# Kernel optimization log

Hardware: AMD Instinct MI355X
Metric: run time of the kernel (lower is better)

The kernel has to match this reference:

```python
import jax, jax.numpy as jnp
import numpy as np

B, L, HID = 2, 2048, 2560
H, HKV, DH = 32, 8, 128
G = H // HKV  # GQA groups = 4
EPS = 1e-6
THETA = 1000000.0


def setup_inputs() -> dict:
    key = jax.random.key(0)
    ks = jax.random.split(key, 6)
    x = jax.random.normal(ks[0], (B, L, HID), dtype=jnp.float32)
    Wq = jax.random.normal(ks[1], (HID, H * DH), dtype=jnp.float32) * 0.02
    Wk = jax.random.normal(ks[2], (HID, HKV * DH), dtype=jnp.float32) * 0.02
    Wv = jax.random.normal(ks[3], (HID, HKV * DH), dtype=jnp.float32) * 0.02
    Wo = jax.random.normal(ks[4], (H * DH, HID), dtype=jnp.float32) * 0.02
    q_norm_w = jnp.ones((DH,), dtype=jnp.float32)
    k_norm_w = jnp.ones((DH,), dtype=jnp.float32)
    # RoPE tables, theta=1e6, non-interleaved (half-split) layout
    inv_freq = 1.0 / (THETA ** (jnp.arange(0, DH, 2, dtype=jnp.float32) / DH))
    pos = jnp.arange(L, dtype=jnp.float32)
    freqs = pos[:, None] * inv_freq[None, :]              # [L, DH/2]
    emb = jnp.concatenate([freqs, freqs], axis=-1)        # [L, DH]
    cos = jnp.broadcast_to(jnp.cos(emb)[None], (B, L, DH))
    sin = jnp.broadcast_to(jnp.sin(emb)[None], (B, L, DH))
    return {"x": x, "Wq": Wq, "Wk": Wk, "Wv": Wv, "Wo": Wo,
            "q_norm_w": q_norm_w, "k_norm_w": k_norm_w,
            "cos": cos, "sin": sin}


def _rmsnorm(x, w):
    xf = x.astype(jnp.float32)
    var = jnp.mean(xf * xf, axis=-1, keepdims=True)
    return (xf * jax.lax.rsqrt(var + EPS)).astype(x.dtype) * w


def _rotate_half(x):
    x1, x2 = jnp.split(x, 2, axis=-1)
    return jnp.concatenate([-x2, x1], axis=-1)


def reference(x, Wq, Wk, Wv, Wo, q_norm_w, k_norm_w, cos, sin):
    b, l, _ = x.shape
    q = (x @ Wq).reshape(b, l, H, DH)
    k = (x @ Wk).reshape(b, l, HKV, DH)
    v = (x @ Wv).reshape(b, l, HKV, DH).transpose(0, 2, 1, 3)   # [B,HKV,L,DH]
    q = _rmsnorm(q, q_norm_w).transpose(0, 2, 1, 3)             # [B,H,L,DH]
    k = _rmsnorm(k, k_norm_w).transpose(0, 2, 1, 3)             # [B,HKV,L,DH]
    c = cos[:, None]  # [B,1,L,DH]
    s = sin[:, None]
    q = q * c + _rotate_half(q) * s
    k = k * c + _rotate_half(k) * s
    # GQA SDPA, causal
    qg = q.reshape(b, HKV, G, l, DH)
    scale = 1.0 / np.sqrt(DH)
    scores = jnp.einsum('bkgqd,bkmd->bkgqm', qg, k) * scale     # [B,HKV,G,L,L]
    causal = jnp.tril(jnp.ones((l, l), dtype=bool))
    scores = jnp.where(causal, scores, jnp.finfo(scores.dtype).min)
    attn = jax.nn.softmax(scores, axis=-1)
    out = jnp.einsum('bkgqm,bkmd->bkgqd', attn, v)              # [B,HKV,G,L,DH]
    out = out.reshape(b, H, l, DH).transpose(0, 2, 1, 3).reshape(b, l, H * DH)
    return out @ Wo
```

## Files before the change

### kernel.cpp

```cpp
#include <hip/hip_runtime.h>

typedef unsigned short u16;
typedef unsigned int u32;
using bf16x8 = __attribute__((ext_vector_type(8))) __bf16;
using f32x4  = __attribute__((ext_vector_type(4))) float;

typedef const void __attribute__((address_space(1)))* gas1p;
typedef void __attribute__((address_space(3)))* las3p;

__device__ __forceinline__ void gload16(const void* g, void* l) {
  __builtin_amdgcn_global_load_lds((gas1p)g, (las3p)l, 16, 0, 0);
}

__device__ __forceinline__ u16 f2bf(float f) {
  union { float f; unsigned u; } v; v.f = f;
  unsigned r = v.u + 0x7FFFu + ((v.u >> 16) & 1u);
  return (u16)(r >> 16);
}
__device__ __forceinline__ float bf2f(u16 h) {
  union { unsigned u; float f; } v; v.u = ((unsigned)h) << 16;
  return v.f;
}

__global__ __launch_bounds__(256)
void cvt_f32_bf16(const float4* __restrict__ in, uint2* __restrict__ out, int n4) {
  int i = blockIdx.x * 256 + threadIdx.x;
  if (i >= n4) return;
  float4 v = in[i];
  uint2 o;
  o.x = (unsigned)f2bf(v.x) | ((unsigned)f2bf(v.y) << 16);
  o.y = (unsigned)f2bf(v.z) | ((unsigned)f2bf(v.w) << 16);
  out[i] = o;
}

__global__ __launch_bounds__(256)
void transpose_all(const float* __restrict__ Wq, const float* __restrict__ Wk,
                   const float* __restrict__ Wv, const float* __restrict__ Wo,
                   u16* __restrict__ WqkvT, u16* __restrict__ WoT) {
  __shared__ float tile[32][33];
  const int bid = blockIdx.x;
  const float* in; u16* out; int C, R, bx, by;
  if (bid < 10240)      { in = Wq; out = WqkvT;                         R = 2560; C = 4096; bx = bid % 128;           by = bid / 128; }
  else if (bid < 12800) { in = Wk; out = WqkvT + (size_t)4096 * 2560;   R = 2560; C = 1024; bx = (bid - 10240) % 32;  by = (bid - 10240) / 32; }
  else if (bid < 15360) { in = Wv; out = WqkvT + (size_t)5120 * 2560;   R = 2560; C = 1024; bx = (bid - 12800) % 32;  by = (bid - 12800) / 32; }
  else                  { in = Wo; out = WoT;                           R = 4096; C = 2560; bx = (bid - 15360) % 80;  by = (bid - 15360) / 80; }
  const int tx = threadIdx.x & 31, ty = threadIdx.x >> 5;
  const int r0 = by * 32, c0 = bx * 32;
#pragma unroll
  for (int i = 0; i < 4; i++)
    tile[ty + i * 8][tx] = in[(size_t)(r0 + ty + i * 8) * C + c0 + tx];
  __syncthreads();
#pragma unroll
  for (int i = 0; i < 4; i++)
    out[(size_t)(c0 + ty + i * 8) * R + r0 + tx] = f2bf(tile[tx][ty + i * 8]);
}

__global__ __launch_bounds__(256)
void transpose_v(const u16* __restrict__ QKV, u16* __restrict__ Vt) {
  __shared__ u16 tile[32][34];
  const int tx = threadIdx.x & 31, ty = threadIdx.x >> 5;
  const int l0 = blockIdx.x * 32, d0 = blockIdx.y * 32;
  const int bkv = blockIdx.z;
  const int b = bkv >> 3, kvh = bkv & 7;
#pragma unroll
  for (int i = 0; i < 4; i++)
    tile[ty + i * 8][tx] =
        QKV[(size_t)(b * 2048 + l0 + ty + i * 8) * 6144 + 5120 + kvh * 128 + d0 + tx];
  __syncthreads();
#pragma unroll
  for (int i = 0; i < 4; i++)
    Vt[((size_t)bkv * 128 + d0 + ty + i * 8) * 2048 + l0 + tx] = tile[tx][ty + i * 8];
}

__global__ __launch_bounds__(256)
void norm_rope(const u16* __restrict__ QKV, const float* __restrict__ qw,
               const float* __restrict__ kw, const float* __restrict__ cosp,
               const float* __restrict__ sinp, u16* __restrict__ Qr,
               u16* __restrict__ Kr) {
  const int rid = blockIdx.x * 4 + (threadIdx.x >> 6);
  const int lane = threadIdx.x & 63;
  const int head = rid % 40;
  const int bl = rid / 40;
  const int b = bl >> 11, l = bl & 2047;
  const u16* src; const float* w; u16* dst; float scale;
  if (head < 32) {
    src = QKV + (size_t)bl * 6144 + head * 128;
    w = qw;
    dst = Qr + ((size_t)(b * 32 + head) * 2048 + l) * 128;
    scale = 0.08838834764831845f;
  } else {
    const int kvh = head - 32;
    src = QKV + (size_t)bl * 6144 + 4096 + kvh * 128;
    w = kw;
    dst = Kr + ((size_t)(b * 8 + kvh) * 2048 + l) * 128;
    scale = 1.0f;
  }
  float lo = bf2f(src[lane]);
  float hi = bf2f(src[lane + 64]);
  float ss = lo * lo + hi * hi;
#pragma unroll
  for (int m = 1; m < 64; m <<= 1) ss += __shfl_xor(ss, m, 64);
  const float rstd = rsqrtf(ss * (1.0f / 128.0f) + 1e-6f) * scale;
  const float nlo = lo * rstd * w[lane];
  const float nhi = hi * rstd * w[lane + 64];
  const float* cb = cosp + (size_t)bl * 128;
  const float* sb = sinp + (size_t)bl * 128;
  dst[lane]      = f2bf(nlo * cb[lane]      - nhi * sb[lane]);
  dst[lane + 64] = f2bf(nhi * cb[lane + 64] + nlo * sb[lane + 64]);
}

#define BAR __builtin_amdgcn_s_barrier()
#define WLG { asm volatile("s_waitcnt lgkmcnt(0)" ::: "memory");            \
              __builtin_amdgcn_sched_barrier(0); }
#define WVMn(n) asm volatile("s_waitcnt vmcnt(" #n ")" ::: "memory")
#define SP1 __builtin_amdgcn_s_setprio(1)
#define SP0 __builtin_amdgcn_s_setprio(0)

template <int MINW, int BM, int BN, int WM, int WN, typename CT>
__global__ __launch_bounds__(512, MINW)
void gemmT(const u16* __restrict__ A, const u16* __restrict__ Bt,
           CT* __restrict__ C, int N, int K, int MT) {
  extern __shared__ char smem[];
  constexpr int ASZ = BM * 128;
  constexpr int BSZ = BN * 128;
  constexpr int MI = BM / WM / 16;
  constexpr int NJF = BN / WN / 16;
  constexpr int NL = BM / 64 + (BN + 63) / 64;
  const int tid = threadIdx.x, lane = tid & 63, wid = tid >> 6;
  const int wm = wid / WN, wn = wid % WN;
  const int fr = lane & 15, fq = lane >> 4;
  const int qx = (int)gridDim.x >> 3;
  const int wg = ((int)blockIdx.x & 7) * qx + ((int)blockIdx.x >> 3);
  const int bx = wg / MT, by = wg - bx * MT;
  const int m0 = by * BM, n0 = bx * BN;
  const u16* Ab = A + (size_t)m0 * K;
  const u16* Bb = Bt + (size_t)n0 * K;

#define ABUF(c) (smem + (c) * ASZ)
#define BBUF(c) (smem + 2 * ASZ + (c) * BSZ)

  f32x4 acc[MI][NJF];
#pragma unroll
  for (int i = 0; i < MI; i++)
#pragma unroll
    for (int j = 0; j < NJF; j++)
#pragma unroll
      for (int r = 0; r < 4; r++) acc[i][j][r] = 0.f;

  auto stage = [&](int c, int kk) {
#pragma unroll
    for (int l = 0; l < BM / 64; l++) {
      const int u = tid + 512 * l, row = u >> 3, ch = u & 7;
      gload16(Ab + (size_t)row * K + ((ch ^ (row & 7)) << 3) + kk,
              ABUF(c) + (u << 4));
    }
#pragma unroll
    for (int l = 0; l < BN / 64; l++) {
      const int u = tid + 512 * l, row = u >> 3, ch = u & 7;
      gload16(Bb + (size_t)row * K + ((ch ^ (row & 7)) << 3) + kk,
              BBUF(c) + (u << 4));
    }
    if constexpr ((BN % 64) != 0) {
      const int u = (BN / 64) * 512 + (tid & 255), row = u >> 3, ch = u & 7;
      gload16(Bb + (size_t)row * K + ((ch ^ (row & 7)) << 3) + kk,
              BBUF(c) + (u << 4));
    }
  };

  const int NT = K >> 6;
  stage(0, 0);
  stage(1, 64);
  if constexpr (NL == 5) { WVMn(5); } else { WVMn(7); }
  BAR;

  bf16x8 af[MI][2], bf[NJF][2];
  for (int t = 0; t < NT; t++) {
    const int c = t & 1;
#pragma unroll
    for (int i = 0; i < MI; i++) {
      const int row = (wm * MI + i) * 16 + fr;
#pragma unroll
      for (int ks = 0; ks < 2; ks++)
        af[i][ks] = *(const bf16x8*)(ABUF(c) + row * 128 +
                                     ((((ks << 2) + fq) ^ (row & 7)) << 4));
    }
#pragma unroll
    for (int j = 0; j < NJF; j++) {
      const int row = (j * WN + wn) * 16 + fr;
#pragma unroll
      for (int ks = 0; ks < 2; ks++)
        bf[j][ks] = *(const bf16x8*)(BBUF(c) + row * 128 +
                                     ((((ks << 2) + fq) ^ (row & 7)) << 4));
    }
    WLG;
    BAR;
    int t2 = t + 2; if (t2 >= NT) t2 -= NT;
    stage(c, t2 << 6);
    if constexpr (NL == 5) { WVMn(5); } else { WVMn(7); }
    SP1;
#pragma unroll
    for (int j = 0; j < NJF; j++)
#pragma unroll
      for (int i = 0; i < MI; i++) {
        acc[i][j] = __builtin_amdgcn_mfma_f32_16x16x32_bf16(af[i][0], bf[j][0],
                                                            acc[i][j], 0, 0, 0);
        acc[i][j] = __builtin_amdgcn_mfma_f32_16x16x32_bf16(af[i][1], bf[j][1],
                                                            acc[i][j], 0, 0, 0);
      }
    SP0;
    BAR;
  }
  WVMn(0);

#pragma unroll
  for (int i = 0; i < MI; i++) {
    const int row0 = m0 + (wm * MI + i) * 16 + fq * 4;
#pragma unroll
    for (int j = 0; j < NJF; j++) {
      const int col = n0 + (j * WN + wn) * 16 + fr;
#pragma unroll
      for (int r = 0; r < 4; r++) {
        const size_t idx = (size_t)(row0 + r) * N + col;
        if constexpr (sizeof(CT) == 2) C[idx] = f2bf(acc[i][j][r]);
        else C[idx] = acc[i][j][r];
      }
    }
  }
#undef ABUF
#undef BBUF
}

__global__ __launch_bounds__(256, 2)
void attn_fwd(const u16* __restrict__ Qr, const u16* __restrict__ Kr,
              const u16* __restrict__ Vt, u16* __restrict__ AO) {
  const int L = 2048, DH = 128;
  __shared__ u16 Ks[2][64 * 128];
  __shared__ u16 Vs[2][128 * 64];
  const int tid = threadIdx.x, lane = tid & 63, wid = tid >> 6;
  const int fr = lane & 15, fq = lane >> 4;
  const int j = blockIdx.x >> 4;
  const int grp = blockIdx.x & 15;
  const int kvh = grp >> 1, b = grp & 1;
  const int h = kvh * 4 + wid;

  const u16* Kbase = Kr + (size_t)(b * 8 + kvh) * L * DH;
  const u16* Vbase = Vt + (size_t)(b * 8 + kvh) * DH * L;

  int Dly[4], kOff[4], vOff[4];
#pragma unroll
  for (int p = 0; p < 4; p++) {
    const int D = (tid + p * 256) * 16;
    Dly[p] = D;
    const int kr = D >> 8, kc = ((D >> 4) & 15) ^ (kr & 7);
    kOff[p] = kr * 128 + kc * 8;
    const int vr = D >> 7, vc = ((D >> 4) & 7) ^ (vr & 7);
    vOff[p] = vr * 2048 + vc * 8;
  }

  auto stage = [&](int kt, int bufi) {
    const int k0 = kt * 64;
#pragma unroll
    for (int p = 0; p < 4; p++) {
      gload16(Kbase + (size_t)k0 * 128 + kOff[p], (char*)&Ks[bufi][0] + Dly[p]);
      gload16(Vbase + k0 + vOff[p], (char*)&Vs[bufi][0] + Dly[p]);
    }
  };

  for (int half = 0; half < 2; half++) {
    const int t = half ? 63 - j : j;
    const int nk = (t >> 1) + 1;

    bf16x8 qf[2][4];
#pragma unroll
    for (int g = 0; g < 2; g++) {
      const int qq = t * 32 + g * 16 + fr;
      const u16* qbase = Qr + ((size_t)(b * 32 + h) * L + qq) * DH + fq * 8;
#pragma unroll
      for (int dt = 0; dt < 4; dt++) qf[g][dt] = *(const bf16x8*)(qbase + dt * 32);
    }
    asm volatile("s_waitcnt vmcnt(0)" ::: "memory");

    f32x4 o[2][8];
#pragma unroll
    for (int g = 0; g < 2; g++)
#pragma unroll
      for (int d = 0; d < 8; d++)
#pragma unroll
        for (int r = 0; r < 4; r++) o[g][d][r] = 0.f;
    float mrow[2] = {-__builtin_huge_valf(), -__builtin_huge_valf()};
    float lrow[2] = {0.f, 0.f};

    __builtin_amdgcn_s_barrier();
    stage(0, 0);
    int cur = 0;

    for (int kt = 0; kt < nk; kt++) {
      if (kt + 1 < nk) {
        stage(kt + 1, cur ^ 1);
        asm volatile("s_waitcnt vmcnt(8)" ::: "memory");
      } else {
        asm volatile("s_waitcnt vmcnt(0)" ::: "memory");
      }
      __builtin_amdgcn_s_barrier();

      const u16* KsB = &Ks[cur][0];
      const u16* VsB = &Vs[cur][0];
      const int k0 = kt * 64;

      f32x4 s4[2][4];
#pragma unroll
      for (int g = 0; g < 2; g++)
#pragma unroll
        for (int ni = 0; ni < 4; ni++)
#pragma unroll
          for (int r = 0; r < 4; r++) s4[g][ni][r] = 0.f;
      SP1;
#pragma unroll
      for (int ni = 0; ni < 4; ni++) {
        const int krow = ni * 16 + fr;
        const int sw = (krow & 7) << 4;
#pragma unroll
        for (int dt = 0; dt < 4; dt++) {
          const int off = (krow * 256 + dt * 64 + fq * 16) ^ sw;
          bf16x8 kf = *(const bf16x8*)((const char*)KsB + off);
          s4[0][ni] = __builtin_amdgcn_mfma_f32_16x16x32_bf16(kf, qf[0][dt], s4[0][ni], 0, 0, 0);
          s4[1][ni] = __builtin_amdgcn_mfma_f32_16x16x32_bf16(kf, qf[1][dt], s4[1][ni], 0, 0, 0);
        }
      }
      SP0;

      if (kt == nk - 1) {
#pragma unroll
        for (int g = 0; g < 2; g++) {
          const int qq = t * 32 + g * 16 + fr;
#pragma unroll
          for (int ni = 0; ni < 4; ni++)
#pragma unroll
            for (int r = 0; r < 4; r++)
              if (k0 + ni * 16 + fq * 4 + r > qq) s4[g][ni][r] = -1e30f;
        }
      }

      bf16x8 pb[2][2];
#pragma unroll
      for (int g = 0; g < 2; g++) {
        float m0t = fmaxf(fmaxf(s4[g][0][0], s4[g][0][1]), fmaxf(s4[g][0][2], s4[g][0][3]));
        float m1t = fmaxf(fmaxf(s4[g][1][0], s4[g][1][1]), fmaxf(s4[g][1][2], s4[g][1][3]));
        float m2t = fmaxf(fmaxf(s4[g][2][0], s4[g][2][1]), fmaxf(s4[g][2][2], s4[g][2][3]));
        float m3t = fmaxf(fmaxf(s4[g][3][0], s4[g][3][1]), fmaxf(s4[g][3][2], s4[g][3][3]));
        float mt = fmaxf(fmaxf(m0t, m1t), fmaxf(m2t, m3t));
        mt = fmaxf(mt, __shfl_xor(mt, 16, 64));
        mt = fmaxf(mt, __shfl_xor(mt, 32, 64));

        if (!__all(mt <= mrow[g] + 8.f)) {
          const float mn = fmaxf(mrow[g], mt);
          const float corr = exp2f((mrow[g] - mn) * 1.44269504f);
          mrow[g] = mn;
          lrow[g] *= corr;
#pragma unroll
          for (int d = 0; d < 8; d++)
#pragma unroll
            for (int r = 0; r < 4; r++) o[g][d][r] *= corr;
        }

        const float ml = mrow[g] * 1.44269504f;
        float rp[4] = {0.f, 0.f, 0.f, 0.f};
#pragma unroll
        for (int ni = 0; ni < 4; ni++)
#pragma unroll
          for (int r = 0; r < 4; r++) {
            const float pv = exp2f(fmaf(s4[g][ni][r], 1.44269504f, -ml));
            s4[g][ni][r] = pv;
            rp[r] += pv;
          }
        float rs = (rp[0] + rp[1]) + (rp[2] + rp[3]);
        rs += __shfl_xor(rs, 16, 64);
        rs += __shfl_xor(rs, 32, 64);
        lrow[g] += rs;

        u32 pk[4][2];
#pragma unroll
        for (int ni = 0; ni < 4; ni++) {
          pk[ni][0] = __builtin_amdgcn_perm(__float_as_uint(s4[g][ni][1]),
                                            __float_as_uint(s4[g][ni][0]), 0x07060302u);
          pk[ni][1] = __builtin_amdgcn_perm(__float_as_uint(s4[g][ni][3]),
                                            __float_as_uint(s4[g][ni][2]), 0x07060302u);
        }
#pragma unroll
        for (int ks = 0; ks < 2; ks++) {
          auto s0 = __builtin_amdgcn_permlane32_swap(pk[2 * ks + 0][0],
                                                     pk[2 * ks + 1][0], false, false);
          auto s1 = __builtin_amdgcn_permlane32_swap(pk[2 * ks + 0][1],
                                                     pk[2 * ks + 1][1], false, false);
          auto q0 = __builtin_amdgcn_permlane16_swap(s0[0], s0[1], false, false);
          auto q1 = __builtin_amdgcn_permlane16_swap(s1[0], s1[1], false, false);
          union { u32 u[4]; bf16x8 v; } pbv;
          pbv.u[0] = q0[0]; pbv.u[1] = q1[0]; pbv.u[2] = q0[1]; pbv.u[3] = q1[1];
          pb[g][ks] = pbv.v;
        }
      }

      SP1;
#pragma unroll
      for (int d = 0; d < 8; d++) {
        const int vrow = d * 16 + fr;
        const int sw = (vrow & 7) << 4;
#pragma unroll
        for (int ks = 0; ks < 2; ks++) {
          const int off = (vrow * 128 + ks * 64 + fq * 16) ^ sw;
          bf16x8 vf = *(const bf16x8*)((const char*)VsB + off);
          o[0][d] = __builtin_amdgcn_mfma_f32_16x16x32_bf16(vf, pb[0][ks], o[0][d], 0, 0, 0);
          o[1][d] = __builtin_amdgcn_mfma_f32_16x16x32_bf16(vf, pb[1][ks], o[1][d], 0, 0, 0);
        }
      }
      SP0;
      __builtin_amdgcn_s_barrier();
      cur ^= 1;
    }

#pragma unroll
    for (int g = 0; g < 2; g++) {
      const float inv = 1.f / lrow[g];
      const int qq = t * 32 + g * 16 + fr;
      u16* obase = AO + ((size_t)b * L + qq) * 4096 + h * 128 + fq * 4;
#pragma unroll
      for (int d = 0; d < 8; d++) {
        uint2 w;
        w.x = (u32)f2bf(o[g][d][0] * inv) | ((u32)f2bf(o[g][d][1] * inv) << 16);
        w.y = (u32)f2bf(o[g][d][2] * inv) | ((u32)f2bf(o[g][d][3] * inv) << 16);
        *(uint2*)(obase + d * 16) = w;
      }
    }
  }
}

extern "C" void kernel_launch(void* const* d_in, const int* in_sizes, int n_in,
                              void* d_out, int out_size, void* d_ws, size_t ws_size,
                              hipStream_t stream) {
  const float* x    = (const float*)d_in[0];
  const float* Wq   = (const float*)d_in[1];
  const float* Wk   = (const float*)d_in[2];
  const float* Wv   = (const float*)d_in[3];
  const float* Wo   = (const float*)d_in[4];
  const float* qw   = (const float*)d_in[5];
  const float* kw   = (const float*)d_in[6];
  const float* cosp = (const float*)d_in[7];
  const float* sinp = (const float*)d_in[8];
  float* out = (float*)d_out;
  char* ws = (char*)d_ws;

  u16* xb    = (u16*)(ws);
  u16* WqkvT = (u16*)(ws + 20971520);
  u16* WoT   = (u16*)(ws + 52428800);
  u16* QKV   = (u16*)(ws + 73400320);
  u16* AO    = QKV;
  u16* Qrr   = (u16*)(ws + 123731968);
  u16* Krr   = (u16*)(ws + 157286400);
  u16* Vtt   = (u16*)(ws + 165675008);

  hipFuncSetAttribute(reinterpret_cast<const void*>(&gemmT<4, 128, 192, 2, 4, u16>),
                      hipFuncAttributeMaxDynamicSharedMemorySize, 81920);
  hipFuncSetAttribute(reinterpret_cast<const void*>(&gemmT<2, 256, 160, 4, 2, float>),
                      hipFuncAttributeMaxDynamicSharedMemorySize, 106496);

  cvt_f32_bf16<<<10240, 256, 0, stream>>>((const float4*)x, (uint2*)xb, 2621440);
  transpose_all<<<25600, 256, 0, stream>>>(Wq, Wk, Wv, Wo, WqkvT, WoT);

  gemmT<4, 128, 192, 2, 4, u16><<<1024, 512, 81920, stream>>>(xb, WqkvT, QKV, 6144, 2560, 32);

  norm_rope<<<40960, 256, 0, stream>>>(QKV, qw, kw, cosp, sinp, Qrr, Krr);
  transpose_v<<<dim3(64, 4, 16), 256, 0, stream>>>(QKV, Vtt);

  attn_fwd<<<dim3(512), 256, 0, stream>>>(Qrr, Krr, Vtt, AO);

  gemmT<2, 256, 160, 4, 2, float><<<256, 512, 106496, stream>>>(AO, WoT, out, 2560, 4096, 16);
}
```

Measured before the change: 408.4 us.

## Split attention into one tile per block, read V directly, retile output GEMM

```diff
diff --git a/kernel.cpp b/kernel.cpp
--- a/kernel.cpp
+++ b/kernel.cpp
@@ -230,206 +230,191 @@
 #undef BBUF
 }
 
-__global__ __launch_bounds__(256, 2)
+__global__ __launch_bounds__(256, 4)
 void attn_fwd(const u16* __restrict__ Qr, const u16* __restrict__ Kr,
               const u16* __restrict__ Vt, u16* __restrict__ AO) {
   const int L = 2048, DH = 128;
   __shared__ u16 Ks[2][64 * 128];
-  __shared__ u16 Vs[2][128 * 64];
   const int tid = threadIdx.x, lane = tid & 63, wid = tid >> 6;
   const int fr = lane & 15, fq = lane >> 4;
-  const int j = blockIdx.x >> 4;
+  const int t = 63 - (int)(blockIdx.x >> 4);
   const int grp = blockIdx.x & 15;
   const int kvh = grp >> 1, b = grp & 1;
   const int h = kvh * 4 + wid;
+  const int nk = (t >> 1) + 1;
 
   const u16* Kbase = Kr + (size_t)(b * 8 + kvh) * L * DH;
   const u16* Vbase = Vt + (size_t)(b * 8 + kvh) * DH * L;
 
-  int Dly[4], kOff[4], vOff[4];
+  int Dly[4], kOff[4];
 #pragma unroll
   for (int p = 0; p < 4; p++) {
     const int D = (tid + p * 256) * 16;
     Dly[p] = D;
     const int kr = D >> 8, kc = ((D >> 4) & 15) ^ (kr & 7);
     kOff[p] = kr * 128 + kc * 8;
-    const int vr = D >> 7, vc = ((D >> 4) & 7) ^ (vr & 7);
-    vOff[p] = vr * 2048 + vc * 8;
-  }
-
-  auto stage = [&](int kt, int bufi) {
+  }
+
+  auto stageK = [&](int kt, int bufi) {
     const int k0 = kt * 64;
 #pragma unroll
-    for (int p = 0; p < 4; p++) {
+    for (int p = 0; p < 4; p++)
       gload16(Kbase + (size_t)k0 * 128 + kOff[p], (char*)&Ks[bufi][0] + Dly[p]);
-      gload16(Vbase + k0 + vOff[p], (char*)&Vs[bufi][0] + Dly[p]);
-    }
   };
 
-  for (int half = 0; half < 2; half++) {
-    const int t = half ? 63 - j : j;
-    const int nk = (t >> 1) + 1;
-
-    bf16x8 qf[2][4];
+  bf16x8 qf[2][4];
+#pragma unroll
+  for (int g = 0; g < 2; g++) {
+    const int qq = t * 32 + g * 16 + fr;
+    const u16* qbase = Qr + ((size_t)(b * 32 + h) * L + qq) * DH + fq * 8;
+#pragma unroll
+    for (int dt = 0; dt < 4; dt++) qf[g][dt] = *(const bf16x8*)(qbase + dt * 32);
+  }
+
+  f32x4 o[2][8];
+#pragma unroll
+  for (int g = 0; g < 2; g++)
+#pragma unroll
+    for (int d = 0; d < 8; d++)
+#pragma unroll
+      for (int r = 0; r < 4; r++) o[g][d][r] = 0.f;
+  float mrow[2] = {-__builtin_huge_valf(), -__builtin_huge_valf()};
+  float lrow[2] = {0.f, 0.f};
+
+  stageK(0, 0);
+  asm volatile("s_waitcnt vmcnt(0)" ::: "memory");
+  __builtin_amdgcn_s_barrier();
+  int cur = 0;
+
+  for (int kt = 0; kt < nk; kt++) {
+    if (kt + 1 < nk) stageK(kt + 1, cur ^ 1);
+
+    const u16* KsB = &Ks[cur][0];
+    const int k0 = kt * 64;
+
+    f32x4 s4[2][4];
+#pragma unroll
+    for (int g = 0; g < 2; g++)
+#pragma unroll
+      for (int ni = 0; ni < 4; ni++)
+#pragma unroll
+        for (int r = 0; r < 4; r++) s4[g][ni][r] = 0.f;
+    SP1;
+#pragma unroll
+    for (int ni = 0; ni < 4; ni++) {
+      const int krow = ni * 16 + fr;
+      const int sw = (krow & 7) << 4;
+#pragma unroll
+      for (int dt = 0; dt < 4; dt++) {
+        const int off = (krow * 256 + dt * 64 + fq * 16) ^ sw;
+        bf16x8 kf = *(const bf16x8*)((const char*)KsB + off);
+        s4[0][ni] = __builtin_amdgcn_mfma_f32_16x16x32_bf16(kf, qf[0][dt], s4[0][ni], 0, 0, 0);
+        s4[1][ni] = __builtin_amdgcn_mfma_f32_16x16x32_bf16(kf, qf[1][dt], s4[1][ni], 0, 0, 0);
+      }
+    }
+    SP0;
+
+    if (kt == nk - 1) {
+#pragma unroll
+      for (int g = 0; g < 2; g++) {
+        const int qq = t * 32 + g * 16 + fr;
+#pragma unroll
+        for (int ni = 0; ni < 4; ni++)
+#pragma unroll
+          for (int r = 0; r < 4; r++)
+            if (k0 + ni * 16 + fq * 4 + r > qq) s4[g][ni][r] = -1e30f;
+      }
+    }
+
+    bf16x8 pb[2][2];
 #pragma unroll
     for (int g = 0; g < 2; g++) {
-      const int qq = t * 32 + g * 16 + fr;
-      const u16* qbase = Qr + ((size_t)(b * 32 + h) * L + qq) * DH + fq * 8;
-#pragma unroll
-      for (int dt = 0; dt < 4; dt++) qf[g][dt] = *(const bf16x8*)(qbase + dt * 32);
-    }
+      float m0t = fmaxf(fmaxf(s4[g][0][0], s4[g][0][1]), fmaxf(s4[g][0][2], s4[g][0][3]));
+      float m1t = fmaxf(fmaxf(s4[g][1][0], s4[g][1][1]), fmaxf(s4[g][1][2], s4[g][1][3]));
+      float m2t = fmaxf(fmaxf(s4[g][2][0], s4[g][2][1]), fmaxf(s4[g][2][2], s4[g][2][3]));
+      float m3t = fmaxf(fmaxf(s4[g][3][0], s4[g][3][1]), fmaxf(s4[g][3][2], s4[g][3][3]));
+      float mt = fmaxf(fmaxf(m0t, m1t), fmaxf(m2t, m3t));
+      mt = fmaxf(mt, __shfl_xor(mt, 16, 64));
+      mt = fmaxf(mt, __shfl_xor(mt, 32, 64));
+
+      if (!__all(mt <= mrow[g] + 8.f)) {
+        const float mn = fmaxf(mrow[g], mt);
+        const float corr = exp2f((mrow[g] - mn) * 1.44269504f);
+        mrow[g] = mn;
+        lrow[g] *= corr;
+#pragma unroll
+        for (int d = 0; d < 8; d++)
+#pragma unroll
+          for (int r = 0; r < 4; r++) o[g][d][r] *= corr;
+      }
+
+      const float ml = mrow[g] * 1.44269504f;
+      float rp[4] = {0.f, 0.f, 0.f, 0.f};
+#pragma unroll
+      for (int ni = 0; ni < 4; ni++)
+#pragma unroll
+        for (int r = 0; r < 4; r++) {
+          const float pv = exp2f(fmaf(s4[g][ni][r], 1.44269504f, -ml));
+          s4[g][ni][r] = pv;
+          rp[r] += pv;
+        }
+      float rs = (rp[0] + rp[1]) + (rp[2] + rp[3]);
+      rs += __shfl_xor(rs, 16, 64);
+      rs += __shfl_xor(rs, 32, 64);
+      lrow[g] += rs;
+
+      u32 pk[4][2];
+#pragma unroll
+      for (int ni = 0; ni < 4; ni++) {
+        pk[ni][0] = __builtin_amdgcn_perm(__float_as_uint(s4[g][ni][1]),
+                                          __float_as_uint(s4[g][ni][0]), 0x07060302u);
+        pk[ni][1] = __builtin_amdgcn_perm(__float_as_uint(s4[g][ni][3]),
+                                          __float_as_uint(s4[g][ni][2]), 0x07060302u);
+      }
+#pragma unroll
+      for (int ks = 0; ks < 2; ks++) {
+        auto s0 = __builtin_amdgcn_permlane32_swap(pk[2 * ks + 0][0],
+                                                   pk[2 * ks + 1][0], false, false);
+        auto s1 = __builtin_amdgcn_permlane32_swap(pk[2 * ks + 0][1],
+                                                   pk[2 * ks + 1][1], false, false);
+        auto q0 = __builtin_amdgcn_permlane16_swap(s0[0], s0[1], false, false);
+        auto q1 = __builtin_amdgcn_permlane16_swap(s1[0], s1[1], false, false);
+        union { u32 u[4]; bf16x8 v; } pbv;
+        pbv.u[0] = q0[0]; pbv.u[1] = q1[0]; pbv.u[2] = q0[1]; pbv.u[3] = q1[1];
+        pb[g][ks] = pbv.v;
+      }
+    }
+
+    const u16* Vk = Vbase + k0;
+    SP1;
+#pragma unroll
+    for (int d = 0; d < 8; d++) {
+      const u16* vrowp = Vk + (size_t)(d * 16 + fr) * L + fq * 8;
+#pragma unroll
+      for (int ks = 0; ks < 2; ks++) {
+        bf16x8 vf = *(const bf16x8*)(vrowp + ks * 32);
+        o[0][d] = __builtin_amdgcn_mfma_f32_16x16x32_bf16(vf, pb[0][ks], o[0][d], 0, 0, 0);
+        o[1][d] = __builtin_amdgcn_mfma_f32_16x16x32_bf16(vf, pb[1][ks], o[1][d], 0, 0, 0);
+      }
+    }
+    SP0;
+
     asm volatile("s_waitcnt vmcnt(0)" ::: "memory");
-
-    f32x4 o[2][8];
-#pragma unroll
-    for (int g = 0; g < 2; g++)
-#pragma unroll
-      for (int d = 0; d < 8; d++)
-#pragma unroll
-        for (int r = 0; r < 4; r++) o[g][d][r] = 0.f;
-    float mrow[2] = {-__builtin_huge_valf(), -__builtin_huge_valf()};
-    float lrow[2] = {0.f, 0.f};
-
     __builtin_amdgcn_s_barrier();
-    stage(0, 0);
-    int cur = 0;
-
-    for (int kt = 0; kt < nk; kt++) {
-      if (kt + 1 < nk) {
-        stage(kt + 1, cur ^ 1);
-        asm volatile("s_waitcnt vmcnt(8)" ::: "memory");
-      } else {
-        asm volatile("s_waitcnt vmcnt(0)" ::: "memory");
-      }
-      __builtin_amdgcn_s_barrier();
-
-      const u16* KsB = &Ks[cur][0];
-      const u16* VsB = &Vs[cur][0];
-      const int k0 = kt * 64;
-
-      f32x4 s4[2][4];
-#pragma unroll
-      for (int g = 0; g < 2; g++)
-#pragma unroll
-        for (int ni = 0; ni < 4; ni++)
-#pragma unroll
-          for (int r = 0; r < 4; r++) s4[g][ni][r] = 0.f;
-      SP1;
-#pragma unroll
-      for (int ni = 0; ni < 4; ni++) {
-        const int krow = ni * 16 + fr;
-        const int sw = (krow & 7) << 4;
-#pragma unroll
-        for (int dt = 0; dt < 4; dt++) {
-          const int off = (krow * 256 + dt * 64 + fq * 16) ^ sw;
-          bf16x8 kf = *(const bf16x8*)((const char*)KsB + off);
-          s4[0][ni] = __builtin_amdgcn_mfma_f32_16x16x32_bf16(kf, qf[0][dt], s4[0][ni], 0, 0, 0);
-          s4[1][ni] = __builtin_amdgcn_mfma_f32_16x16x32_bf16(kf, qf[1][dt], s4[1][ni], 0, 0, 0);
-        }
-      }
-      SP0;
-
-      if (kt == nk - 1) {
-#pragma unroll
-        for (int g = 0; g < 2; g++) {
-          const int qq = t * 32 + g * 16 + fr;
-#pragma unroll
-          for (int ni = 0; ni < 4; ni++)
-#pragma unroll
-            for (int r = 0; r < 4; r++)
-              if (k0 + ni * 16 + fq * 4 + r > qq) s4[g][ni][r] = -1e30f;
-        }
-      }
-
-      bf16x8 pb[2][2];
-#pragma unroll
-      for (int g = 0; g < 2; g++) {
-        float m0t = fmaxf(fmaxf(s4[g][0][0], s4[g][0][1]), fmaxf(s4[g][0][2], s4[g][0][3]));
-        float m1t = fmaxf(fmaxf(s4[g][1][0], s4[g][1][1]), fmaxf(s4[g][1][2], s4[g][1][3]));
-        float m2t = fmaxf(fmaxf(s4[g][2][0], s4[g][2][1]), fmaxf(s4[g][2][2], s4[g][2][3]));
-        float m3t = fmaxf(fmaxf(s4[g][3][0], s4[g][3][1]), fmaxf(s4[g][3][2], s4[g][3][3]));
-        float mt = fmaxf(fmaxf(m0t, m1t), fmaxf(m2t, m3t));
-        mt = fmaxf(mt, __shfl_xor(mt, 16, 64));
-        mt = fmaxf(mt, __shfl_xor(mt, 32, 64));
-
-        if (!__all(mt <= mrow[g] + 8.f)) {
-          const float mn = fmaxf(mrow[g], mt);
-          const float corr = exp2f((mrow[g] - mn) * 1.44269504f);
-          mrow[g] = mn;
-          lrow[g] *= corr;
-#pragma unroll
-          for (int d = 0; d < 8; d++)
-#pragma unroll
-            for (int r = 0; r < 4; r++) o[g][d][r] *= corr;
-        }
-
-        const float ml = mrow[g] * 1.44269504f;
-        float rp[4] = {0.f, 0.f, 0.f, 0.f};
-#pragma unroll
-        for (int ni = 0; ni < 4; ni++)
-#pragma unroll
-          for (int r = 0; r < 4; r++) {
-            const float pv = exp2f(fmaf(s4[g][ni][r], 1.44269504f, -ml));
-            s4[g][ni][r] = pv;
-            rp[r] += pv;
-          }
-        float rs = (rp[0] + rp[1]) + (rp[2] + rp[3]);
-        rs += __shfl_xor(rs, 16, 64);
-        rs += __shfl_xor(rs, 32, 64);
-        lrow[g] += rs;
-
-        u32 pk[4][2];
-#pragma unroll
-        for (int ni = 0; ni < 4; ni++) {
-          pk[ni][0] = __builtin_amdgcn_perm(__float_as_uint(s4[g][ni][1]),
-                                            __float_as_uint(s4[g][ni][0]), 0x07060302u);
-          pk[ni][1] = __builtin_amdgcn_perm(__float_as_uint(s4[g][ni][3]),
-                                            __float_as_uint(s4[g][ni][2]), 0x07060302u);
-        }
-#pragma unroll
-        for (int ks = 0; ks < 2; ks++) {
-          auto s0 = __builtin_amdgcn_permlane32_swap(pk[2 * ks + 0][0],
-                                                     pk[2 * ks + 1][0], false, false);
-          auto s1 = __builtin_amdgcn_permlane32_swap(pk[2 * ks + 0][1],
-                                                     pk[2 * ks + 1][1], false, false);
-          auto q0 = __builtin_amdgcn_permlane16_swap(s0[0], s0[1], false, false);
-          auto q1 = __builtin_amdgcn_permlane16_swap(s1[0], s1[1], false, false);
-          union { u32 u[4]; bf16x8 v; } pbv;
-          pbv.u[0] = q0[0]; pbv.u[1] = q1[0]; pbv.u[2] = q0[1]; pbv.u[3] = q1[1];
-          pb[g][ks] = pbv.v;
-        }
-      }
-
-      SP1;
-#pragma unroll
-      for (int d = 0; d < 8; d++) {
-        const int vrow = d * 16 + fr;
-        const int sw = (vrow & 7) << 4;
-#pragma unroll
-        for (int ks = 0; ks < 2; ks++) {
-          const int off = (vrow * 128 + ks * 64 + fq * 16) ^ sw;
-          bf16x8 vf = *(const bf16x8*)((const char*)VsB + off);
-          o[0][d] = __builtin_amdgcn_mfma_f32_16x16x32_bf16(vf, pb[0][ks], o[0][d], 0, 0, 0);
-          o[1][d] = __builtin_amdgcn_mfma_f32_16x16x32_bf16(vf, pb[1][ks], o[1][d], 0, 0, 0);
-        }
-      }
-      SP0;
-      __builtin_amdgcn_s_barrier();
-      cur ^= 1;
-    }
-
-#pragma unroll
-    for (int g = 0; g < 2; g++) {
-      const float inv = 1.f / lrow[g];
-      const int qq = t * 32 + g * 16 + fr;
-      u16* obase = AO + ((size_t)b * L + qq) * 4096 + h * 128 + fq * 4;
-#pragma unroll
-      for (int d = 0; d < 8; d++) {
-        uint2 w;
-        w.x = (u32)f2bf(o[g][d][0] * inv) | ((u32)f2bf(o[g][d][1] * inv) << 16);
-        w.y = (u32)f2bf(o[g][d][2] * inv) | ((u32)f2bf(o[g][d][3] * inv) << 16);
-        *(uint2*)(obase + d * 16) = w;
-      }
+    cur ^= 1;
+  }
+
+#pragma unroll
+  for (int g = 0; g < 2; g++) {
+    const float inv = 1.f / lrow[g];
+    const int qq = t * 32 + g * 16 + fr;
+    u16* obase = AO + ((size_t)b * L + qq) * 4096 + h * 128 + fq * 4;
+#pragma unroll
+    for (int d = 0; d < 8; d++) {
+      uint2 w;
+      w.x = (u32)f2bf(o[g][d][0] * inv) | ((u32)f2bf(o[g][d][1] * inv) << 16);
+      w.y = (u32)f2bf(o[g][d][2] * inv) | ((u32)f2bf(o[g][d][3] * inv) << 16);
+      *(uint2*)(obase + d * 16) = w;
     }
   }
 }
@@ -460,8 +445,8 @@
 
   hipFuncSetAttribute(reinterpret_cast<const void*>(&gemmT<4, 128, 192, 2, 4, u16>),
                       hipFuncAttributeMaxDynamicSharedMemorySize, 81920);
-  hipFuncSetAttribute(reinterpret_cast<const void*>(&gemmT<2, 256, 160, 4, 2, float>),
-                      hipFuncAttributeMaxDynamicSharedMemorySize, 106496);
+  hipFuncSetAttribute(reinterpret_cast<const void*>(&gemmT<4, 128, 160, 4, 2, float>),
+                      hipFuncAttributeMaxDynamicSharedMemorySize, 73728);
 
   cvt_f32_bf16<<<10240, 256, 0, stream>>>((const float4*)x, (uint2*)xb, 2621440);
   transpose_all<<<25600, 256, 0, stream>>>(Wq, Wk, Wv, Wo, WqkvT, WoT);
@@ -471,7 +456,7 @@
   norm_rope<<<40960, 256, 0, stream>>>(QKV, qw, kw, cosp, sinp, Qrr, Krr);
   transpose_v<<<dim3(64, 4, 16), 256, 0, stream>>>(QKV, Vtt);
 
-  attn_fwd<<<dim3(512), 256, 0, stream>>>(Qrr, Krr, Vtt, AO);
-
-  gemmT<2, 256, 160, 4, 2, float><<<256, 512, 106496, stream>>>(AO, WoT, out, 2560, 4096, 16);
-}
+  attn_fwd<<<dim3(1024), 256, 0, stream>>>(Qrr, Krr, Vtt, AO);
+
+  gemmT<4, 128, 160, 4, 2, float><<<512, 512, 73728, stream>>>(AO, WoT, out, 2560, 4096, 32);
+}
```

Measured after the change: 742.7 us. +81.9%, slower.
